# Performance work log

Measured on AMD Instinct MI355X. Metric: run time of the kernel, lower is better.

Reference implementation:

```python
import jax, jax.numpy as jnp
import numpy as np
from jax import lax

B, S, T = 512, 1024, 64


def setup_inputs() -> dict:
    key = jax.random.key(0)
    k1, k2, k3 = jax.random.split(key, 3)
    emissions = jax.random.normal(k1, (B, S, T), dtype=jnp.float32)
    tags = jax.random.randint(k2, (B, S), 0, T)
    mask = jnp.ones((B, S), dtype=jnp.float32)
    transitions = jax.random.uniform(k3, (T, T), dtype=jnp.float32, minval=-0.1, maxval=0.1)
    return {"emissions": emissions, "tags": tags, "mask": mask, "transitions": transitions}


def _partition(emissions, mask, transitions):
    # Faithful to compute_partition: dp starts at zeros and the i=0 step
    # already adds transitions (quirk of the original code).
    def step(dp, xs):
        e_t, m_t = xs  # e_t: [B, T], m_t: [B]
        # scores[b, i, j] = dp[b, i] + transitions[i, j] + e_t[b, j]
        scores = dp[:, :, None] + transitions[None, :, :] + e_t[:, None, :]
        dp_t = jax.nn.logsumexp(scores, axis=1)  # [B, T]
        m = m_t[:, None]
        return m * dp_t + (1.0 - m) * dp, None

    dp0 = jnp.zeros((emissions.shape[0], emissions.shape[2]), dtype=emissions.dtype)
    dp, _ = lax.scan(step, dp0, (jnp.swapaxes(emissions, 0, 1), mask.T))
    return jax.nn.logsumexp(dp, axis=1)  # [B]


def _gold_scores(emissions, tags, mask, transitions):
    # Faithful to compute_scores: sum over t=1..S-1 of (emit_t + trans_t) * mask_t
    emit = jnp.take_along_axis(emissions, tags[..., None], axis=2)[..., 0]  # [B, S]
    trans = transitions[tags[:, :-1], tags[:, 1:]]  # [B, S-1]
    return jnp.sum((emit[:, 1:] + trans) * mask[:, 1:], axis=1)  # [B]


def reference(emissions, tags, mask, transitions):
    z = _partition(emissions, mask, transitions)
    scores = _gold_scores(emissions, tags, mask, transitions)
    return -jnp.mean(z - scores)
```

## Files before the change

### kernel.cpp

```cpp
#include <hip/hip_runtime.h>

#define BATCH 512
#define SEQ   1024
#define NT    64
#define NSEG  8
#define SEGLEN (SEQ / NSEG)
#define NCHG  (SEGLEN / 4)

typedef float    f32x4 __attribute__((ext_vector_type(4)));
typedef _Float16 v8h   __attribute__((ext_vector_type(8)));
typedef _Float16 h2v   __attribute__((ext_vector_type(2)));
typedef int      int4v __attribute__((ext_vector_type(4)));

__device__ __forceinline__ int pkrtz_bits(float a, float b) {
    auto pk = __builtin_amdgcn_cvt_pkrtz(a, b);
    return __builtin_bit_cast(int, pk);
}
__device__ __forceinline__ float exp2_hw(float x) {
    float r; asm("v_exp_f32 %0, %1" : "=v"(r) : "v"(x)); return r;
}
__device__ __forceinline__ float log2_hw(float x) {
    float r; asm("v_log_f32 %0, %1" : "=v"(r) : "v"(x)); return r;
}
#define DPP_MAX(x, ctrl) { int _t = __builtin_amdgcn_update_dpp( \
    __builtin_bit_cast(int,(x)), __builtin_bit_cast(int,(x)), (ctrl), 0xf, 0xf, false); \
    (x) = fmaxf((x), __builtin_bit_cast(float,_t)); }
#define DPP_ADD(x, ctrl) { int _t = __builtin_amdgcn_update_dpp( \
    __builtin_bit_cast(int,(x)), __builtin_bit_cast(int,(x)), (ctrl), 0xf, 0xf, false); \
    (x) += __builtin_bit_cast(float,_t); }

#define GLDS16(gsrc, ldst) \
    __builtin_amdgcn_global_load_lds( \
        (const __attribute__((address_space(1))) unsigned int*)(gsrc), \
        (__attribute__((address_space(3))) unsigned int*)(ldst), 16, 0, 0)
#define GLDS4(gsrc, ldst) \
    __builtin_amdgcn_global_load_lds( \
        (const __attribute__((address_space(1))) unsigned int*)(gsrc), \
        (__attribute__((address_space(3))) unsigned int*)(ldst), 4, 0, 0)

__global__ __launch_bounds__(512, 1) void crf_kernel(
        const float* __restrict__ emis,
        const int*   __restrict__ tags,
        const float* __restrict__ mask,
        const float* __restrict__ trans,
        float*       __restrict__ out)
{
    const int b   = blockIdx.x;
    const int tid = threadIdx.x;
    const int seg = tid >> 6;
    const int l   = tid & 63;
    const int cc  = l & 15;
    const int q   = l >> 4;

    __shared__ float etile[NSEG][4][256];
    __shared__ float mtile[NSEG][SEGLEN];
    __shared__ float ubuf[NT];
    __shared__ float gred[NSEG];
    __shared__ float sigma_sh;

    if (tid < NT) ubuf[tid] = 1.0f;
    if (tid == 0) sigma_sh = 0.0f;

    const float INVLN2 = 1.44269504088896340736f;
    const float LN2    = 0.69314718055994530942f;
    const float KGOV   = 10.26f;
    const f32x4 zero4  = {0.f, 0.f, 0.f, 0.f};

    v8h A0[4][2];
    #pragma unroll
    for (int mt = 0; mt < 4; ++mt) {
        #pragma unroll
        for (int h = 0; h < 2; ++h) {
            int4v pv;
            #pragma unroll
            for (int r2 = 0; r2 < 4; ++r2) {
                const int row0 = 16 * (2*h + (r2 >> 1)) + 4*q + 2*(r2 & 1);
                const int colm = 16 * mt + cc;
                pv[r2] = pkrtz_bits(__expf(trans[row0 * NT + colm]),
                                    __expf(trans[(row0 + 1) * NT + colm]));
            }
            A0[mt][h] = __builtin_bit_cast(v8h, pv);
        }
    }

    v8h Bf[4][2];
    #pragma unroll
    for (int v = 0; v < 4; ++v) {
        #pragma unroll
        for (int h = 0; h < 2; ++h) {
            int4v pv;
            #pragma unroll
            for (int r2 = 0; r2 < 4; ++r2) {
                const int row0 = 16 * (2*h + (r2 >> 1)) + 4*q + 2*(r2 & 1);
                const int col  = 4 * cc + v;
                unsigned lo = (row0 == col)     ? 0x3C00u : 0u;
                unsigned hi = (row0 + 1 == col) ? 0x3C00u : 0u;
                pv[r2] = (int)(lo | (hi << 16));
            }
            Bf[v][h] = __builtin_bit_cast(v8h, pv);
        }
    }

    const float* ebase = emis + (size_t)b * SEQ * NT + (size_t)seg * SEGLEN * NT;
    const float* mbase = mask + (size_t)b * SEQ + seg * SEGLEN;
    const float* etbl  = &etile[seg][0][0];

    GLDS16(ebase + l * 4,       &etile[seg][0][0]);
    GLDS16(ebase + 256 + l * 4, &etile[seg][1][0]);
    GLDS4(mbase + l,      &mtile[seg][0]);
    GLDS4(mbase + 64 + l, &mtile[seg][64]);
    asm volatile("s_waitcnt vmcnt(0)" ::: "memory");

    float ls = 0.0f, mlog1 = 0.0f, rs_use = KGOV;
    f32x4 dA4[4], dB4[4];
    #pragma unroll
    for (int mt = 0; mt < 4; ++mt) {
        const f32x4 ev0 = *(const f32x4*)(etbl + 16*mt + 4*q);
        #pragma unroll
        for (int rr = 0; rr < 4; ++rr)
            dA4[mt][rr] = exp2_hw(fmaf(ev0[rr], INVLN2, -KGOV));
    }

#define STEP(DIN, DOUT, TS) { \
    f32x4 acc_[4][4]; \
    _Pragma("unroll") \
    for (int mt = 0; mt < 4; ++mt) { \
        _Pragma("unroll") \
        for (int v = 0; v < 4; ++v) \
            acc_[mt][v] = __builtin_amdgcn_mfma_f32_16x16x32_f16(A0[mt][1], Bf[v][1], \
                          __builtin_amdgcn_mfma_f32_16x16x32_f16(A0[mt][0], Bf[v][0], zero4, 0,0,0), 0,0,0); \
    } \
    const float rsF = fmaf(0.5f, mlog1, KGOV); \
    { const float* evp_ = etbl + (((g + (((TS)+1) >> 2)) & 3) * 256) + ((((TS)+1) & 3) * 64) + 4*q; \
      _Pragma("unroll") \
      for (int mt = 0; mt < 4; ++mt) { \
          const f32x4 ev_ = *(const f32x4*)(evp_ + 16*mt); \
          _Pragma("unroll") \
          for (int rr = 0; rr < 4; ++rr) \
              DOUT[mt][rr] = exp2_hw(fmaf(ev_[rr], INVLN2, -rsF)); } } \
    _Pragma("unroll") \
    for (int mt = 0; mt < 4; ++mt) { \
        _Pragma("unroll") \
        for (int v = 0; v < 4; ++v) \
            acc_[mt][v] *= DIN[mt]; \
    } \
    const float mk_ = mk4[TS]; \
    if (!a1_ && mk_ != 1.0f) { \
        const float g2_ = exp2_hw(-rs_use), om_ = 1.0f - mk_; \
        _Pragma("unroll") \
        for (int v = 0; v < 4; ++v) { \
            _Pragma("unroll") \
            for (int h = 0; h < 2; ++h) { \
                const int4v bb_ = __builtin_bit_cast(int4v, Bf[v][h]); \
                _Pragma("unroll") \
                for (int r2 = 0; r2 < 4; ++r2) { \
                    const int mt_ = 2*h + (r2 >> 1), rr_ = 2*(r2 & 1); \
                    const h2v gh_ = __builtin_bit_cast(h2v, bb_[r2]); \
                    acc_[mt_][v][rr_]   = mk_ * acc_[mt_][v][rr_]   + om_ * g2_ * (float)gh_.x; \
                    acc_[mt_][v][rr_+1] = mk_ * acc_[mt_][v][rr_+1] + om_ * g2_ * (float)gh_.y; \
                } } } } \
    f32x4 mx_ = acc_[0][0]; \
    _Pragma("unroll") \
    for (int rr = 0; rr < 4; ++rr) mx_[rr] = fmaxf(mx_[rr], acc_[0][1][rr]); \
    _Pragma("unroll") \
    for (int mt = 1; mt < 4; ++mt) { \
        _Pragma("unroll") \
        for (int rr = 0; rr < 4; ++rr) \
            mx_[rr] = fmaxf(mx_[rr], fmaxf(acc_[mt][0][rr], acc_[mt][1][rr])); } \
    float M_ = fmaxf(fmaxf(mx_[0], mx_[1]), fmaxf(mx_[2], mx_[3])); \
    DPP_MAX(M_, 0x128) DPP_MAX(M_, 0x124) DPP_MAX(M_, 0x122) DPP_MAX(M_, 0x121) \
    M_ = fmaxf(M_, __shfl_xor(M_, 16, 64)); \
    M_ = fmaxf(M_, __shfl_xor(M_, 32, 64)); \
    ls += rs_use; rs_use = rsF; mlog1 = log2_hw(M_); \
    _Pragma("unroll") \
    for (int v = 0; v < 4; ++v) { \
        _Pragma("unroll") \
        for (int h = 0; h < 2; ++h) { \
            int4v nb_; \
            _Pragma("unroll") \
            for (int r2 = 0; r2 < 4; ++r2) { \
                const int mt_ = 2*h + (r2 >> 1), rr_ = 2*(r2 & 1); \
                nb_[r2] = pkrtz_bits(acc_[mt_][v][rr_], acc_[mt_][v][rr_+1]); } \
            Bf[v][h] = __builtin_bit_cast(v8h, nb_); } } }

    #pragma unroll 1
    for (int g = 0; g < NCHG; ++g) {
        if (g + 2 < NCHG) {
            GLDS16(ebase + (g + 2) * 256 + l * 4, &etile[seg][(g + 2) & 3][0]);
            asm volatile("s_waitcnt vmcnt(1)" ::: "memory");
        } else {
            asm volatile("s_waitcnt vmcnt(0)" ::: "memory");
        }
        const f32x4 mk4 = *(const f32x4*)&mtile[seg][4 * g];
        const bool a1_ = (mk4[0] == 1.0f) & (mk4[1] == 1.0f) &
                         (mk4[2] == 1.0f) & (mk4[3] == 1.0f);
        STEP(dA4, dB4, 0) STEP(dB4, dA4, 1) STEP(dA4, dB4, 2) STEP(dB4, dA4, 3)
    }

    {
        const int*   tb  = tags + (size_t)b * SEQ;
        const float* ebm = emis + (size_t)b * SEQ * NT;
        const float* mbm = mask + (size_t)b * SEQ;
        float acg = 0.0f;
        for (int s = 1 + tid; s < SEQ; s += NSEG * 64) {
            const int tc = tb[s];
            const int tp = tb[s - 1];
            acg += (ebm[(size_t)s * NT + tc] + trans[tp * NT + tc]) * mbm[s];
        }
        acg += __shfl_xor(acg, 32, 64); acg += __shfl_xor(acg, 16, 64);
        acg += __shfl_xor(acg,  8, 64); acg += __shfl_xor(acg,  4, 64);
        acg += __shfl_xor(acg,  2, 64); acg += __shfl_xor(acg,  1, 64);
        if (l == 0) gred[seg] = acg;
    }

    #pragma unroll 1
    for (int s = 0; s < NSEG; ++s) {
        __syncthreads();
        if (seg == s) {
            float u4[4];
            #pragma unroll
            for (int v = 0; v < 4; ++v) u4[v] = ubuf[4*cc + v];
            float p[16];
            #pragma unroll
            for (int h = 0; h < 2; ++h) {
                #pragma unroll
                for (int e = 0; e < 8; ++e) {
                    float a2 = 0.0f;
                    #pragma unroll
                    for (int v = 0; v < 4; ++v)
                        a2 = fmaf((float)Bf[v][h][e], u4[v], a2);
                    p[h*8 + e] = a2;
                }
            }
            #pragma unroll
            for (int i = 0; i < 16; ++i) {
                DPP_ADD(p[i], 0x128) DPP_ADD(p[i], 0x124)
                DPP_ADD(p[i], 0x122) DPP_ADD(p[i], 0x121)
            }
            float pm = p[0];
            #pragma unroll
            for (int i = 1; i < 16; ++i) pm = fmaxf(pm, p[i]);
            pm = fmaxf(pm, __shfl_xor(pm, 16, 64));
            pm = fmaxf(pm, __shfl_xor(pm, 32, 64));
            const float rpm = 1.0f / pm;
            if (cc == 0) {
                #pragma unroll
                for (int h = 0; h < 2; ++h)
                    #pragma unroll
                    for (int e = 0; e < 8; ++e)
                        ubuf[16*(2*h + (e>>2)) + 4*q + (e&3)] = p[h*8 + e] * rpm;
            }
            if (l == 0) sigma_sh += log2_hw(pm) + ls;
        }
    }
    __syncthreads();

    if (seg == 0) {
        float su = ubuf[l];
        su += __shfl_xor(su, 32, 64); su += __shfl_xor(su, 16, 64);
        su += __shfl_xor(su,  8, 64); su += __shfl_xor(su,  4, 64);
        su += __shfl_xor(su,  2, 64); su += __shfl_xor(su,  1, 64);
        const float Z = LN2 * (sigma_sh + log2_hw(su));
        float gold = 0.0f;
        #pragma unroll
        for (int s = 0; s < NSEG; ++s) gold += gred[s];
        if (l == 0)
            atomicAdd(out, (gold - Z) * (1.0f / BATCH));
    }
}

__global__ void zero_kernel(float* out) { if (threadIdx.x == 0) out[0] = 0.0f; }

extern "C" void kernel_launch(void* const* d_in, const int* in_sizes, int n_in,
                              void* d_out, int out_size, void* d_ws, size_t ws_size,
                              hipStream_t stream) {
    const float* emis  = (const float*)d_in[0];
    const int*   tags  = (const int*)d_in[1];
    const float* mask  = (const float*)d_in[2];
    const float* trans = (const float*)d_in[3];
    float* out = (float*)d_out;

    zero_kernel<<<1, 64, 0, stream>>>(out);
    crf_kernel<<<BATCH, NSEG * 64, 0, stream>>>(emis, tags, mask, trans, out);
}
```

Before: 453.6 us.

## Split each segment's column block across two waves with exponent-based rescaling

```diff
diff --git a/kernel.cpp b/kernel.cpp
--- a/kernel.cpp
+++ b/kernel.cpp
@@ -3,7 +3,7 @@
 #define BATCH 512
 #define SEQ   1024
 #define NT    64
-#define NSEG  8
+#define NSEG  4
 #define SEGLEN (SEQ / NSEG)
 #define NCHG  (SEGLEN / 4)
 
@@ -22,9 +22,9 @@
 __device__ __forceinline__ float log2_hw(float x) {
     float r; asm("v_log_f32 %0, %1" : "=v"(r) : "v"(x)); return r;
 }
-#define DPP_MAX(x, ctrl) { int _t = __builtin_amdgcn_update_dpp( \
-    __builtin_bit_cast(int,(x)), __builtin_bit_cast(int,(x)), (ctrl), 0xf, 0xf, false); \
-    (x) = fmaxf((x), __builtin_bit_cast(float,_t)); }
+__device__ __forceinline__ int frexp_exp_hw(float x) {
+    int r; asm("v_frexp_exp_i32_f32 %0, %1" : "=v"(r) : "v"(x)); return r;
+}
 #define DPP_ADD(x, ctrl) { int _t = __builtin_amdgcn_update_dpp( \
     __builtin_bit_cast(int,(x)), __builtin_bit_cast(int,(x)), (ctrl), 0xf, 0xf, false); \
     (x) += __builtin_bit_cast(float,_t); }
@@ -38,7 +38,7 @@
         (const __attribute__((address_space(1))) unsigned int*)(gsrc), \
         (__attribute__((address_space(3))) unsigned int*)(ldst), 4, 0, 0)
 
-__global__ __launch_bounds__(512, 1) void crf_kernel(
+__global__ __launch_bounds__(512, 4) void crf_kernel(
         const float* __restrict__ emis,
         const int*   __restrict__ tags,
         const float* __restrict__ mask,
@@ -47,15 +47,19 @@
 {
     const int b   = blockIdx.x;
     const int tid = threadIdx.x;
-    const int seg = tid >> 6;
+    const int w   = tid >> 6;
+    const int seg = w >> 1;
+    const int hf  = w & 1;
     const int l   = tid & 63;
     const int cc  = l & 15;
     const int q   = l >> 4;
 
-    __shared__ float etile[NSEG][4][256];
-    __shared__ float mtile[NSEG][SEGLEN];
+    __shared__ float ering[8][4][256];
+    __shared__ float mtile[8][256];
+    __shared__ float ph[2][NT];
     __shared__ float ubuf[NT];
-    __shared__ float gred[NSEG];
+    __shared__ float lsw[8];
+    __shared__ float gredw[8];
     __shared__ float sigma_sh;
 
     if (tid < NT) ubuf[tid] = 1.0f;
@@ -63,8 +67,18 @@
 
     const float INVLN2 = 1.44269504088896340736f;
     const float LN2    = 0.69314718055994530942f;
-    const float KGOV   = 10.26f;
+    const float CBASE  = 6.4f;
     const f32x4 zero4  = {0.f, 0.f, 0.f, 0.f};
+
+    const float* ebase = emis + (size_t)b * SEQ * NT + (size_t)seg * SEGLEN * NT;
+    const float* mbase = mask + (size_t)b * SEQ + seg * SEGLEN;
+
+    GLDS4(mbase + l,       &mtile[w][0]);
+    GLDS4(mbase + 64 + l,  &mtile[w][64]);
+    GLDS4(mbase + 128 + l, &mtile[w][128]);
+    GLDS4(mbase + 192 + l, &mtile[w][192]);
+    GLDS16(ebase + 4 * l,       &ering[w][0][0]);
+    GLDS16(ebase + 256 + 4 * l, &ering[w][1][0]);
 
     v8h A0[4][2];
     #pragma unroll
@@ -83,126 +97,100 @@
         }
     }
 
-    v8h Bf[4][2];
+    v8h Bf[2][2];
     #pragma unroll
-    for (int v = 0; v < 4; ++v) {
+    for (int vt = 0; vt < 2; ++vt) {
         #pragma unroll
         for (int h = 0; h < 2; ++h) {
             int4v pv;
             #pragma unroll
             for (int r2 = 0; r2 < 4; ++r2) {
                 const int row0 = 16 * (2*h + (r2 >> 1)) + 4*q + 2*(r2 & 1);
-                const int col  = 4 * cc + v;
+                const int col  = 4 * cc + 2*hf + vt;
                 unsigned lo = (row0 == col)     ? 0x3C00u : 0u;
                 unsigned hi = (row0 + 1 == col) ? 0x3C00u : 0u;
                 pv[r2] = (int)(lo | (hi << 16));
             }
-            Bf[v][h] = __builtin_bit_cast(v8h, pv);
-        }
-    }
-
-    const float* ebase = emis + (size_t)b * SEQ * NT + (size_t)seg * SEGLEN * NT;
-    const float* mbase = mask + (size_t)b * SEQ + seg * SEGLEN;
-    const float* etbl  = &etile[seg][0][0];
-
-    GLDS16(ebase + l * 4,       &etile[seg][0][0]);
-    GLDS16(ebase + 256 + l * 4, &etile[seg][1][0]);
-    GLDS4(mbase + l,      &mtile[seg][0]);
-    GLDS4(mbase + 64 + l, &mtile[seg][64]);
-    asm volatile("s_waitcnt vmcnt(0)" ::: "memory");
-
-    float ls = 0.0f, mlog1 = 0.0f, rs_use = KGOV;
-    f32x4 dA4[4], dB4[4];
-    #pragma unroll
-    for (int mt = 0; mt < 4; ++mt) {
-        const f32x4 ev0 = *(const f32x4*)(etbl + 16*mt + 4*q);
-        #pragma unroll
-        for (int rr = 0; rr < 4; ++rr)
-            dA4[mt][rr] = exp2_hw(fmaf(ev0[rr], INVLN2, -KGOV));
-    }
-
-#define STEP(DIN, DOUT, TS) { \
-    f32x4 acc_[4][4]; \
+            Bf[vt][h] = __builtin_bit_cast(v8h, pv);
+        }
+    }
+
+    asm volatile("s_waitcnt vmcnt(1)" ::: "memory");
+
+    float ls = 0.0f, exlag1 = 0.0f, exlag2 = 0.0f;
+
+#define STEP(EP, G, TS) { \
+    const float rs = fmaf(0.5f, exlag2, CBASE); \
+    ls += rs; \
+    int dup[4]; \
     _Pragma("unroll") \
     for (int mt = 0; mt < 4; ++mt) { \
-        _Pragma("unroll") \
-        for (int v = 0; v < 4; ++v) \
-            acc_[mt][v] = __builtin_amdgcn_mfma_f32_16x16x32_f16(A0[mt][1], Bf[v][1], \
-                          __builtin_amdgcn_mfma_f32_16x16x32_f16(A0[mt][0], Bf[v][0], zero4, 0,0,0), 0,0,0); \
+        const float ev = (EP)[(TS)*64 + 16*mt + cc]; \
+        const float d  = exp2_hw(fmaf(ev, INVLN2, -rs)); \
+        dup[mt] = pkrtz_bits(d, d); \
     } \
-    const float rsF = fmaf(0.5f, mlog1, KGOV); \
-    { const float* evp_ = etbl + (((g + (((TS)+1) >> 2)) & 3) * 256) + ((((TS)+1) & 3) * 64) + 4*q; \
-      _Pragma("unroll") \
-      for (int mt = 0; mt < 4; ++mt) { \
-          const f32x4 ev_ = *(const f32x4*)(evp_ + 16*mt); \
-          _Pragma("unroll") \
-          for (int rr = 0; rr < 4; ++rr) \
-              DOUT[mt][rr] = exp2_hw(fmaf(ev_[rr], INVLN2, -rsF)); } } \
+    f32x4 acc[4][2]; \
     _Pragma("unroll") \
     for (int mt = 0; mt < 4; ++mt) { \
+        int4v sq = { dup[mt], dup[mt], dup[mt], dup[mt] }; \
+        const v8h dv  = __builtin_bit_cast(v8h, sq); \
+        const v8h As0 = A0[mt][0] * dv; \
+        const v8h As1 = A0[mt][1] * dv; \
         _Pragma("unroll") \
-        for (int v = 0; v < 4; ++v) \
-            acc_[mt][v] *= DIN[mt]; \
+        for (int vt = 0; vt < 2; ++vt) \
+            acc[mt][vt] = __builtin_amdgcn_mfma_f32_16x16x32_f16(As1, Bf[vt][1], \
+                          __builtin_amdgcn_mfma_f32_16x16x32_f16(As0, Bf[vt][0], zero4, 0,0,0), 0,0,0); \
     } \
-    const float mk_ = mk4[TS]; \
-    if (!a1_ && mk_ != 1.0f) { \
-        const float g2_ = exp2_hw(-rs_use), om_ = 1.0f - mk_; \
+    const int exi = frexp_exp_hw(acc[0][0][0]); \
+    const float exf = (float)__builtin_amdgcn_readfirstlane(exi); \
+    exlag2 = exlag1; exlag1 = exf; \
+    const float mk = mtile[w][4*(G) + (TS)]; \
+    if (mk != 1.0f) { \
+        const float g2 = exp2_hw(-rs), om = 1.0f - mk; \
         _Pragma("unroll") \
-        for (int v = 0; v < 4; ++v) { \
+        for (int vt = 0; vt < 2; ++vt) { \
             _Pragma("unroll") \
             for (int h = 0; h < 2; ++h) { \
-                const int4v bb_ = __builtin_bit_cast(int4v, Bf[v][h]); \
+                const int4v bb = __builtin_bit_cast(int4v, Bf[vt][h]); \
                 _Pragma("unroll") \
                 for (int r2 = 0; r2 < 4; ++r2) { \
                     const int mt_ = 2*h + (r2 >> 1), rr_ = 2*(r2 & 1); \
-                    const h2v gh_ = __builtin_bit_cast(h2v, bb_[r2]); \
-                    acc_[mt_][v][rr_]   = mk_ * acc_[mt_][v][rr_]   + om_ * g2_ * (float)gh_.x; \
-                    acc_[mt_][v][rr_+1] = mk_ * acc_[mt_][v][rr_+1] + om_ * g2_ * (float)gh_.y; \
+                    const h2v gh = __builtin_bit_cast(h2v, bb[r2]); \
+                    acc[mt_][vt][rr_]   = mk * acc[mt_][vt][rr_]   + om * g2 * (float)gh.x; \
+                    acc[mt_][vt][rr_+1] = mk * acc[mt_][vt][rr_+1] + om * g2 * (float)gh.y; \
                 } } } } \
-    f32x4 mx_ = acc_[0][0]; \
     _Pragma("unroll") \
-    for (int rr = 0; rr < 4; ++rr) mx_[rr] = fmaxf(mx_[rr], acc_[0][1][rr]); \
-    _Pragma("unroll") \
-    for (int mt = 1; mt < 4; ++mt) { \
-        _Pragma("unroll") \
-        for (int rr = 0; rr < 4; ++rr) \
-            mx_[rr] = fmaxf(mx_[rr], fmaxf(acc_[mt][0][rr], acc_[mt][1][rr])); } \
-    float M_ = fmaxf(fmaxf(mx_[0], mx_[1]), fmaxf(mx_[2], mx_[3])); \
-    DPP_MAX(M_, 0x128) DPP_MAX(M_, 0x124) DPP_MAX(M_, 0x122) DPP_MAX(M_, 0x121) \
-    M_ = fmaxf(M_, __shfl_xor(M_, 16, 64)); \
-    M_ = fmaxf(M_, __shfl_xor(M_, 32, 64)); \
-    ls += rs_use; rs_use = rsF; mlog1 = log2_hw(M_); \
-    _Pragma("unroll") \
-    for (int v = 0; v < 4; ++v) { \
+    for (int vt = 0; vt < 2; ++vt) { \
         _Pragma("unroll") \
         for (int h = 0; h < 2; ++h) { \
-            int4v nb_; \
+            int4v nb; \
             _Pragma("unroll") \
             for (int r2 = 0; r2 < 4; ++r2) { \
                 const int mt_ = 2*h + (r2 >> 1), rr_ = 2*(r2 & 1); \
-                nb_[r2] = pkrtz_bits(acc_[mt_][v][rr_], acc_[mt_][v][rr_+1]); } \
-            Bf[v][h] = __builtin_bit_cast(v8h, nb_); } } }
+                nb[r2] = pkrtz_bits(acc[mt_][vt][rr_], acc[mt_][vt][rr_+1]); \
+            } \
+            Bf[vt][h] = __builtin_bit_cast(v8h, nb); } } }
 
     #pragma unroll 1
     for (int g = 0; g < NCHG; ++g) {
         if (g + 2 < NCHG) {
-            GLDS16(ebase + (g + 2) * 256 + l * 4, &etile[seg][(g + 2) & 3][0]);
-            asm volatile("s_waitcnt vmcnt(1)" ::: "memory");
+            GLDS16(ebase + (g + 2) * 256 + 4 * l, &ering[w][(g + 2) & 3][0]);
+            asm volatile("s_waitcnt vmcnt(2)" ::: "memory");
         } else {
             asm volatile("s_waitcnt vmcnt(0)" ::: "memory");
         }
-        const f32x4 mk4 = *(const f32x4*)&mtile[seg][4 * g];
-        const bool a1_ = (mk4[0] == 1.0f) & (mk4[1] == 1.0f) &
-                         (mk4[2] == 1.0f) & (mk4[3] == 1.0f);
-        STEP(dA4, dB4, 0) STEP(dB4, dA4, 1) STEP(dA4, dB4, 2) STEP(dB4, dA4, 3)
-    }
+        const float* ep = &ering[w][g & 3][0];
+        STEP(ep, g, 0) STEP(ep, g, 1) STEP(ep, g, 2) STEP(ep, g, 3)
+    }
+
+    if (l == 0) lsw[w] = ls;
 
     {
         const int*   tb  = tags + (size_t)b * SEQ;
         const float* ebm = emis + (size_t)b * SEQ * NT;
         const float* mbm = mask + (size_t)b * SEQ;
         float acg = 0.0f;
-        for (int s = 1 + tid; s < SEQ; s += NSEG * 64) {
+        for (int s = 1 + tid; s < SEQ; s += 512) {
             const int tc = tb[s];
             const int tp = tb[s - 1];
             acg += (ebm[(size_t)s * NT + tc] + trans[tp * NT + tc]) * mbm[s];
@@ -210,26 +198,23 @@
         acg += __shfl_xor(acg, 32, 64); acg += __shfl_xor(acg, 16, 64);
         acg += __shfl_xor(acg,  8, 64); acg += __shfl_xor(acg,  4, 64);
         acg += __shfl_xor(acg,  2, 64); acg += __shfl_xor(acg,  1, 64);
-        if (l == 0) gred[seg] = acg;
-    }
+        if (l == 0) gredw[w] = acg;
+    }
+    __syncthreads();
 
     #pragma unroll 1
     for (int s = 0; s < NSEG; ++s) {
-        __syncthreads();
         if (seg == s) {
-            float u4[4];
-            #pragma unroll
-            for (int v = 0; v < 4; ++v) u4[v] = ubuf[4*cc + v];
+            float u4[2];
+            #pragma unroll
+            for (int vt = 0; vt < 2; ++vt) u4[vt] = ubuf[4*cc + 2*hf + vt];
             float p[16];
             #pragma unroll
             for (int h = 0; h < 2; ++h) {
                 #pragma unroll
                 for (int e = 0; e < 8; ++e) {
-                    float a2 = 0.0f;
-                    #pragma unroll
-                    for (int v = 0; v < 4; ++v)
-                        a2 = fmaf((float)Bf[v][h][e], u4[v], a2);
-                    p[h*8 + e] = a2;
+                    p[h*8 + e] = fmaf((float)Bf[0][h][e], u4[0],
+                                      (float)Bf[1][h][e] * u4[1]);
                 }
             }
             #pragma unroll
@@ -237,25 +222,29 @@
                 DPP_ADD(p[i], 0x128) DPP_ADD(p[i], 0x124)
                 DPP_ADD(p[i], 0x122) DPP_ADD(p[i], 0x121)
             }
-            float pm = p[0];
-            #pragma unroll
-            for (int i = 1; i < 16; ++i) pm = fmaxf(pm, p[i]);
-            pm = fmaxf(pm, __shfl_xor(pm, 16, 64));
-            pm = fmaxf(pm, __shfl_xor(pm, 32, 64));
-            const float rpm = 1.0f / pm;
             if (cc == 0) {
                 #pragma unroll
                 for (int h = 0; h < 2; ++h)
                     #pragma unroll
                     for (int e = 0; e < 8; ++e)
-                        ubuf[16*(2*h + (e>>2)) + 4*q + (e&3)] = p[h*8 + e] * rpm;
-            }
-            if (l == 0) sigma_sh += log2_hw(pm) + ls;
-        }
-    }
-    __syncthreads();
-
-    if (seg == 0) {
+                        ph[hf][16*(2*h + (e>>2)) + 4*q + (e&3)] = p[h*8 + e];
+            }
+        }
+        __syncthreads();
+        if (w == 2*s) {
+            const float dlt = lsw[2*s] - lsw[2*s + 1];
+            float val = fmaf(exp2_hw(dlt), ph[1][l], ph[0][l]);
+            float pm = val;
+            pm = fmaxf(pm, __shfl_xor(pm, 32, 64)); pm = fmaxf(pm, __shfl_xor(pm, 16, 64));
+            pm = fmaxf(pm, __shfl_xor(pm,  8, 64)); pm = fmaxf(pm, __shfl_xor(pm,  4, 64));
+            pm = fmaxf(pm, __shfl_xor(pm,  2, 64)); pm = fmaxf(pm, __shfl_xor(pm,  1, 64));
+            ubuf[l] = val / pm;
+            if (l == 0) sigma_sh += lsw[2*s] + log2_hw(pm);
+        }
+        __syncthreads();
+    }
+
+    if (w == 0) {
         float su = ubuf[l];
         su += __shfl_xor(su, 32, 64); su += __shfl_xor(su, 16, 64);
         su += __shfl_xor(su,  8, 64); su += __shfl_xor(su,  4, 64);
@@ -263,7 +252,7 @@
         const float Z = LN2 * (sigma_sh + log2_hw(su));
         float gold = 0.0f;
         #pragma unroll
-        for (int s = 0; s < NSEG; ++s) gold += gred[s];
+        for (int ww = 0; ww < 8; ++ww) gold += gredw[ww];
         if (l == 0)
             atomicAdd(out, (gold - Z) * (1.0f / BATCH));
     }
@@ -281,5 +270,5 @@
     float* out = (float*)d_out;
 
     zero_kernel<<<1, 64, 0, stream>>>(out);
-    crf_kernel<<<BATCH, NSEG * 64, 0, stream>>>(emis, tags, mask, trans, out);
-}
+    crf_kernel<<<BATCH, 512, 0, stream>>>(emis, tags, mask, trans, out);
+}
```

Result: faster. 392.1 us (-13.6%).
